# Performance work log

Hardware: AMD Instinct MI355X
Metric: run time of the kernel (lower is better)

## Reference

```python
import jax, jax.numpy as jnp
import numpy as np

B, T = 512, 512
NQ, K, M, DK, DV, DF = 1000, 5, 50, 64, 256, 50
ABILITY_SCALE = 3.0


def setup_inputs() -> dict:
    key = jax.random.key(0)
    ks = jax.random.split(key, 16)
    s = 0.05
    p = {}
    p["q_data"] = jax.random.randint(ks[0], (B, T), 0, NQ + 1)
    p["r_data"] = jax.random.randint(ks[1], (B, T), 0, K)
    p["q_embed_W"] = jax.random.normal(ks[2], (NQ + 1, DK)) * s
    p["Mk"] = jax.random.normal(ks[3], (M, DK)) * s
    p["Mv0"] = jax.random.normal(ks[4], (M, DV)) * s
    p["value_W"] = jax.random.normal(ks[5], (2 * NQ, DV)) * s
    p["value_b"] = jnp.zeros((DV,))
    p["erase_W"] = jax.random.normal(ks[6], (DV, DV)) * s
    p["erase_b"] = jnp.zeros((DV,))
    p["add_W"] = jax.random.normal(ks[7], (DV, DV)) * s
    p["add_b"] = jnp.zeros((DV,))
    p["summary_W"] = jax.random.normal(ks[8], (DV + DK, DF)) * s
    p["summary_b"] = jnp.zeros((DF,))
    p["ability_W"] = jax.random.normal(ks[9], (DF, 1)) * s
    p["ability_b"] = jnp.zeros((1,))
    p["thresh_W"] = jax.random.normal(ks[10], (DK, K - 1)) * s
    p["thresh_b"] = jnp.zeros((K - 1,))
    p["disc_W"] = jax.random.normal(ks[11], (DF + DK, 1)) * s
    p["disc_b"] = jnp.zeros((1,))
    p["corn_W"] = jax.random.normal(ks[12], (DF + DK, K - 1)) * s
    p["corn_b"] = jnp.zeros((K - 1,))
    return p


def reference(q_data, r_data, q_embed_W, Mk, Mv0, value_W, value_b, erase_W, erase_b,
              add_W, add_b, summary_W, summary_b, ability_W, ability_b,
              thresh_W, thresh_b, disc_W, disc_b, corn_W, corn_b):
    nq = value_W.shape[0] // 2
    k_cats = corn_W.shape[1] + 1
    b = q_data.shape[0]
    qe = q_embed_W[q_data]                                # [B,T,DK] question key embedding
    valid = (q_data > 0)[..., None]                       # q==0 is padding (one-hot col dropped)
    idx = jnp.maximum(q_data - 1, 0)
    # ordered embedding [one_hot(q), (r/(K-1))*one_hot(q)] @ value_W == exact row gather
    rs = r_data.astype(qe.dtype) / (k_cats - 1)
    ve = value_W[idx] + rs[..., None] * value_W[nq + idx]
    ve = jnp.where(valid, ve, 0.0) + value_b              # [B,T,DV]
    # attention over key memory (time-independent, hoisted out of the recurrence)
    w = jax.nn.softmax(jnp.einsum('btk,mk->btm', qe, Mk), axis=-1)  # [B,T,M]
    erase = jax.nn.sigmoid(ve @ erase_W + erase_b)        # [B,T,DV]
    add = jnp.tanh(ve @ add_W + add_b)                    # [B,T,DV]
    Mv_init = jnp.broadcast_to(Mv0, (b,) + Mv0.shape)     # [B,M,DV]

    def step(Mv, inp):
        w_t, e_t, a_t = inp                               # [B,M], [B,DV], [B,DV]
        read = jnp.einsum('bm,bmv->bv', w_t, Mv)          # read BEFORE write (t reads state < t)
        Mv = Mv * (1.0 - w_t[:, :, None] * e_t[:, None, :]) + w_t[:, :, None] * a_t[:, None, :]
        return Mv, read

    _, reads = jax.lax.scan(step, Mv_init,
                            (jnp.swapaxes(w, 0, 1), jnp.swapaxes(erase, 0, 1), jnp.swapaxes(add, 0, 1)))
    reads = jnp.swapaxes(reads, 0, 1)                     # [B,T,DV]

    summary = jnp.tanh(jnp.concatenate([reads, qe], -1) @ summary_W + summary_b)  # [B,T,DF]
    theta = (summary @ ability_W + ability_b)[..., 0] * ABILITY_SCALE             # [B,T]
    betas = qe @ thresh_W + thresh_b                                              # [B,T,K-1]
    di = jnp.concatenate([summary, qe], -1)                                       # [B,T,DF+DK]
    alpha = jax.nn.softplus(di @ disc_W + disc_b)[..., 0]                         # [B,T]
    logits = di @ corn_W + corn_b                                                 # [B,T,K-1]
    # CORN: cumulative conditional probs -> class probabilities
    cp = jnp.cumprod(jax.nn.sigmoid(logits), axis=-1)     # P(y > k)
    upper = jnp.concatenate([jnp.ones_like(cp[..., :1]), cp], -1)
    lower = jnp.concatenate([cp, jnp.zeros_like(cp[..., :1])], -1)
    probs = upper - lower                                 # [B,T,K]
    return theta, betas, alpha, probs, logits
```

## Files before the change

### kernel.cpp

```cpp
#include <hip/hip_runtime.h>

typedef unsigned short u16;
typedef unsigned int u32;
typedef __bf16 bf16x8 __attribute__((ext_vector_type(8)));
typedef float fx4 __attribute__((ext_vector_type(4)));
typedef float fx2 __attribute__((ext_vector_type(2)));

#define NT 262144
#define B_SZ 512
#define T_LEN 512
#define NQv 1000
#define VE_ROWS 5120
#define TLP 264
#define SSP 53

__device__ __forceinline__ float bf2f(u16 u) { return __uint_as_float(((u32)u) << 16); }
__device__ __forceinline__ u16 f2bf(float f) {
    u32 x = __float_as_uint(f);
    x += 0x7fffu + ((x >> 16) & 1u);
    return (u16)(x >> 16);
}
__device__ __forceinline__ u32 pack2(float a, float b) {
    return (u32)f2bf(a) | ((u32)f2bf(b) << 16);
}
__device__ __forceinline__ float sigm(float x) { return 1.0f / (1.0f + __expf(-x)); }
__device__ __forceinline__ float tanh_fast(float x) {
    float e2 = __expf(2.0f * x);
    return 1.0f - 2.0f / (e2 + 1.0f);
}
__device__ __forceinline__ void load_lds16(const void* g, void* l) {
    __builtin_amdgcn_global_load_lds(
        (const __attribute__((address_space(1))) u32*)g,
        (__attribute__((address_space(3))) u32*)l, 16, 0, 0);
}

__global__ __launch_bounds__(256) void k_prep_w(const float* __restrict__ eW,
                                                const float* __restrict__ aW,
                                                const float* __restrict__ sW,
                                                u16* __restrict__ Wt,
                                                u16* __restrict__ SWt) {
    int id = blockIdx.x * 256 + threadIdx.x;
    if (id < 131072) {
        int n = id >> 8, k = id & 255;
        Wt[n * 256 + k] = f2bf((n < 256) ? eW[k * 256 + n] : aW[k * 256 + (n - 256)]);
    } else {
        int id2 = id - 131072;
        if (id2 < 16384) {
            int n = id2 >> 8, k = id2 & 255;
            SWt[n * 256 + k] = (n < 50) ? f2bf(sW[k * 50 + n]) : (u16)0;
        }
    }
}

__global__ __launch_bounds__(256) void k_w_tab(const float* __restrict__ qeW,
                                               const float* __restrict__ Mk,
                                               float* __restrict__ w_tab) {
    __shared__ __align__(16) float mk[3200];
    int tid = threadIdx.x;
    for (int i = tid; i < 3200; i += 256) mk[i] = Mk[i];
    int q = blockIdx.x * 256 + tid;
    __syncthreads();
    if (q > NQv) return;

    float qe[64];
    {
        const float4* qr = (const float4*)(qeW + (size_t)q * 64);
#pragma unroll
        for (int i = 0; i < 16; i++) {
            float4 u = qr[i];
            qe[4 * i + 0] = u.x; qe[4 * i + 1] = u.y;
            qe[4 * i + 2] = u.z; qe[4 * i + 3] = u.w;
        }
    }
    float lg[50];
#pragma unroll
    for (int m = 0; m < 50; m++) {
        const float* mr = &mk[m * 64];
        float acc = 0.f;
#pragma unroll
        for (int k = 0; k < 64; k++) acc = fmaf(qe[k], mr[k], acc);
        lg[m] = acc;
    }
    float mx = -1e30f;
#pragma unroll
    for (int m = 0; m < 50; m++) mx = fmaxf(mx, lg[m]);
    float sum = 0.f;
#pragma unroll
    for (int m = 0; m < 50; m++) { lg[m] = __expf(lg[m] - mx); sum += lg[m]; }
    float inv = 1.0f / sum;
#pragma unroll
    for (int m = 0; m < 50; m++) w_tab[(size_t)q * 50 + m] = lg[m] * inv;
}

__global__ __launch_bounds__(256) void k_ve_tab(const float* __restrict__ vW,
                                                const float* __restrict__ vb,
                                                u16* __restrict__ ve_tab) {
    int id = blockIdx.x * 256 + threadIdx.x;
    int row = id >> 5, seg = id & 31;
    if (row >= VE_ROWS) return;
    int q = row / 5;
    int r = row - q * 5;
    if (q > NQv) q = NQv;
    int idx = (q > 0) ? (q - 1) : 0;
    float rs = (float)r * 0.25f;
    float vf = (q > 0) ? 1.0f : 0.0f;

    const float* pa = vW + (size_t)idx * 256 + seg * 8;
    const float* pb = pa + NQv * 256;
    float4 a0 = ((const float4*)pa)[0];
    float4 a1 = ((const float4*)pa)[1];
    float4 b0 = ((const float4*)pb)[0];
    float4 b1 = ((const float4*)pb)[1];
    const float* vbp = vb + seg * 8;
    float o0 = vf * fmaf(rs, b0.x, a0.x) + vbp[0];
    float o1 = vf * fmaf(rs, b0.y, a0.y) + vbp[1];
    float o2 = vf * fmaf(rs, b0.z, a0.z) + vbp[2];
    float o3 = vf * fmaf(rs, b0.w, a0.w) + vbp[3];
    float o4 = vf * fmaf(rs, b1.x, a1.x) + vbp[4];
    float o5 = vf * fmaf(rs, b1.y, a1.y) + vbp[5];
    float o6 = vf * fmaf(rs, b1.z, a1.z) + vbp[6];
    float o7 = vf * fmaf(rs, b1.w, a1.w) + vbp[7];
    uint4 o;
    o.x = pack2(o0, o1); o.y = pack2(o2, o3);
    o.z = pack2(o4, o5); o.w = pack2(o6, o7);
    *(uint4*)(ve_tab + (size_t)row * 256 + seg * 8) = o;
}

__global__ __launch_bounds__(256) void k_q_tabs(const float* __restrict__ qeW,
                                                const float* __restrict__ sW,
                                                const float* __restrict__ tW,
                                                const float* __restrict__ tb,
                                                const float* __restrict__ dW,
                                                const float* __restrict__ cW,
                                                float* __restrict__ sq_tab,
                                                float* __restrict__ beta_tab,
                                                float* __restrict__ dq_tab,
                                                float* __restrict__ cq_tab) {
    int id = blockIdx.x * 256 + threadIdx.x;
    int q = id >> 6, n = id & 63;
    if (q > NQv) return;
    float qe[64];
    const float4* qr = (const float4*)(qeW + (size_t)q * 64);
#pragma unroll
    for (int i = 0; i < 16; i++) {
        float4 u = qr[i];
        qe[4 * i + 0] = u.x; qe[4 * i + 1] = u.y;
        qe[4 * i + 2] = u.z; qe[4 * i + 3] = u.w;
    }
    if (n < 50) {
        float acc = 0.f;
#pragma unroll
        for (int k = 0; k < 64; k++) acc = fmaf(qe[k], sW[(256 + k) * 50 + n], acc);
        sq_tab[(size_t)q * 50 + n] = acc;
    } else if (n < 54) {
        int j = n - 50;
        float acc = tb[j];
#pragma unroll
        for (int k = 0; k < 64; k++) acc = fmaf(qe[k], tW[k * 4 + j], acc);
        beta_tab[(size_t)q * 4 + j] = acc;
    } else if (n == 54) {
        float acc = 0.f;
#pragma unroll
        for (int k = 0; k < 64; k++) acc = fmaf(qe[k], dW[50 + k], acc);
        dq_tab[q] = acc;
    } else if (n >= 56 && n < 60) {
        int j = n - 56;
        float acc = 0.f;
#pragma unroll
        for (int k = 0; k < 64; k++) acc = fmaf(qe[k], cW[(50 + k) * 4 + j], acc);
        cq_tab[(size_t)q * 4 + j] = acc;
    }
}

__global__ __launch_bounds__(256) void k_gemm_ea(const u16* __restrict__ ve,
                                                 const u16* __restrict__ Wt,
                                                 const float* __restrict__ eb,
                                                 const float* __restrict__ ab,
                                                 u16* __restrict__ e_out,
                                                 u16* __restrict__ a_out) {
    __shared__ __align__(16) u16 smem[8192];
    u16* lA = smem;
    u16* lB = smem + 4096;

    int tid = threadIdx.x;
    int row0 = blockIdx.x * 128;
    int col0 = blockIdx.y * 128;

    int wave = tid >> 6, lane = tid & 63;
    int wm = wave >> 1, wn = wave & 1;
    int rl = lane & 15, quad = lane >> 4;
    fx4 acc[4][4] = {};

    int c0 = tid, c1 = tid + 256;
    int r0_ = c0 >> 2, j0 = c0 & 3;
    int r1_ = c1 >> 2, j1 = c1 & 3;

    for (int k0 = 0; k0 < 256; k0 += 32) {
        load_lds16(ve + (size_t)(row0 + r0_) * 256 + k0 + j0 * 8, lA + c0 * 8);
        load_lds16(ve + (size_t)(row0 + r1_) * 256 + k0 + j1 * 8, lA + c1 * 8);
        load_lds16(Wt + (size_t)(col0 + r0_) * 256 + k0 + j0 * 8, lB + c0 * 8);
        load_lds16(Wt + (size_t)(col0 + r1_) * 256 + k0 + j1 * 8, lB + c1 * 8);
        __syncthreads();
        bf16x8 af[4], bfr[4];
#pragma unroll
        for (int i = 0; i < 4; i++) af[i] = *(const bf16x8*)(lA + (wm * 64 + i * 16 + rl) * 32 + quad * 8);
#pragma unroll
        for (int j = 0; j < 4; j++) bfr[j] = *(const bf16x8*)(lB + (wn * 64 + j * 16 + rl) * 32 + quad * 8);
#pragma unroll
        for (int i = 0; i < 4; i++)
#pragma unroll
            for (int j = 0; j < 4; j++)
                acc[i][j] = __builtin_amdgcn_mfma_f32_16x16x32_bf16(af[i], bfr[j], acc[i][j], 0, 0, 0);
        __syncthreads();
    }

    bool is_er = (col0 < 256);
    const float* bias = is_er ? eb : ab;
    u16* outp = is_er ? e_out : a_out;
    int cb0 = col0 & 255;
    u16* cst = smem;
#pragma unroll
    for (int h = 0; h < 2; h++) {
        if (wm == h) {
#pragma unroll
            for (int j = 0; j < 4; j++) {
                int nl = wn * 64 + j * 16 + rl;
                float bv = bias[cb0 + nl];
#pragma unroll
                for (int i = 0; i < 4; i++) {
                    int rowl = i * 16 + quad * 4;
#pragma unroll
                    for (int r = 0; r < 4; r++) {
                        float x = acc[i][j][r] + bv;
                        cst[(rowl + r) * 128 + nl] = f2bf(is_er ? sigm(x) : tanh_fast(x));
                    }
                }
            }
        }
        __syncthreads();
#pragma unroll
        for (int c = 0; c < 4; c++) {
            int idx = c * 256 + tid;
            int row = idx >> 4, seg = idx & 15;
            *(uint4*)(outp + (size_t)(row0 + h * 64 + row) * 256 + cb0 + seg * 8) =
                *(const uint4*)(cst + row * 128 + seg * 8);
        }
        __syncthreads();
    }
}

__global__ __launch_bounds__(256) void k_fused(const int* __restrict__ q_data,
                                               const int* __restrict__ r_data,
                                               const float* __restrict__ w_tab,
                                               const u16* __restrict__ e_tab,
                                               const u16* __restrict__ a_tab,
                                               const float* __restrict__ Mv0,
                                               const u16* __restrict__ SWt,
                                               const float* __restrict__ sq_tab,
                                               const float* __restrict__ sb,
                                               const float* __restrict__ abilW,
                                               const float* __restrict__ abilb,
                                               const float* __restrict__ beta_tab,
                                               const float* __restrict__ dW,
                                               const float* __restrict__ db,
                                               const float* __restrict__ dq_tab,
                                               const float* __restrict__ cW,
                                               const float* __restrict__ cb,
                                               const float* __restrict__ cq_tab,
                                               float* __restrict__ out) {
    int b = blockIdx.x;
    int tid = threadIdx.x;
    __shared__ __align__(16) u16 tileA[128 * TLP];
    __shared__ float wls[2][8][52];
    __shared__ int sq_idx[128];

    const int* qp = q_data + (size_t)b * T_LEN;
    const int* rp = r_data + (size_t)b * T_LEN;

    int wave = tid >> 6, lane = tid & 63;
    int wm = wave >> 1, wn = wave & 1;
    int rl = lane & 15, quad = lane >> 4;

    fx2 Mv[25];
#pragma unroll
    for (int i = 0; i < 25; i++) {
        Mv[i].x = Mv0[(2 * i) * 256 + tid];
        Mv[i].y = Mv0[(2 * i + 1) * 256 + tid];
    }

    u16 eu[8], au[8];
#pragma unroll
    for (int s = 0; s < 8; s++) {
        int qr = qp[s] * 5 + rp[s];
        eu[s] = e_tab[(size_t)qr * 256 + tid];
        au[s] = a_tab[(size_t)qr * 256 + tid];
    }
    if (tid < 200) {
        int s = tid / 25, m2 = tid % 25;
        float2 w0 = ((const float2*)(w_tab + (size_t)qp[s] * 50))[m2];
        wls[0][s][2 * m2] = w0.x;
        wls[0][s][2 * m2 + 1] = w0.y;
    }
    __syncthreads();

    const int ngrp = T_LEN / 8;
    for (int g = 0; g < ngrp; g++) {
        int cur = g & 1, nxt = cur ^ 1;
        bool has_next = (g + 1 < ngrp);
        int tn0 = (g + 1) * 8;

        u16 eun[8], aun[8];
        float2 wn_ = make_float2(0.f, 0.f);
        if (has_next) {
#pragma unroll
            for (int s = 0; s < 8; s++) {
                int qr = qp[tn0 + s] * 5 + rp[tn0 + s];
                eun[s] = e_tab[(size_t)qr * 256 + tid];
                aun[s] = a_tab[(size_t)qr * 256 + tid];
            }
            if (tid < 200) {
                int s = tid / 25, m2 = tid % 25;
                wn_ = ((const float2*)(w_tab + (size_t)qp[tn0 + s] * 50))[m2];
            }
        }

#pragma unroll
        for (int s = 0; s < 8; s++) {
            float e = bf2f(eu[s]), a = bf2f(au[s]);
            fx2 e2; e2.x = e; e2.y = e;
            fx2 a2; a2.x = a; a2.y = a;
            const fx2* wv = (const fx2*)&wls[cur][s][0];
            fx2 rd2; rd2.x = 0.f; rd2.y = 0.f;
#pragma unroll
            for (int i = 0; i < 25; i++) {
                fx2 w2 = wv[i];
                rd2 = rd2 + w2 * Mv[i];
                fx2 t2 = a2 - e2 * Mv[i];
                Mv[i] = Mv[i] + w2 * t2;
            }
            int tokrow = (g * 8 + s) & 127;
            tileA[tokrow * TLP + tid] = f2bf(rd2.x + rd2.y);
        }

        if (has_next) {
            if (tid < 200) {
                int s = tid / 25, m2 = tid % 25;
                wls[nxt][s][2 * m2] = wn_.x;
                wls[nxt][s][2 * m2 + 1] = wn_.y;
            }
#pragma unroll
            for (int s = 0; s < 8; s++) { eu[s] = eun[s]; au[s] = aun[s]; }
        }
        __syncthreads();

        if ((g & 15) == 15) {
            int tile0 = (g >> 4) * 128;
            if (tid < 128) sq_idx[tid] = qp[tile0 + tid];

            fx4 acc[4][2] = {};
#pragma unroll
            for (int ks = 0; ks < 8; ks++) {
                int k0 = ks * 32;
                bf16x8 af[4], bfr[2];
#pragma unroll
                for (int i = 0; i < 4; i++)
                    af[i] = *(const bf16x8*)(tileA + (wm * 64 + i * 16 + rl) * TLP + k0 + quad * 8);
#pragma unroll
                for (int j = 0; j < 2; j++)
                    bfr[j] = *(const bf16x8*)(SWt + (size_t)(wn * 32 + j * 16 + rl) * 256 + k0 + quad * 8);
#pragma unroll
                for (int i = 0; i < 4; i++)
#pragma unroll
                    for (int j = 0; j < 2; j++)
                        acc[i][j] = __builtin_amdgcn_mfma_f32_16x16x32_bf16(af[i], bfr[j], acc[i][j], 0, 0, 0);
            }
            __syncthreads();

            float* sS = (float*)tileA;
#pragma unroll
            for (int j = 0; j < 2; j++) {
                int n = wn * 32 + j * 16 + rl;
                if (n < 50) {
#pragma unroll
                    for (int i = 0; i < 4; i++) {
                        int rowl = wm * 64 + i * 16 + quad * 4;
#pragma unroll
                        for (int r = 0; r < 4; r++)
                            sS[(rowl + r) * SSP + n] = acc[i][j][r];
                    }
                }
            }
            __syncthreads();

            if (tid < 128) {
                int q = sq_idx[tid];
                size_t gtok = (size_t)b * T_LEN + tile0 + tid;
                const float* sq = sq_tab + (size_t)q * 50;
                const float* sp = sS + tid * SSP;

                float th = abilb[0];
                float da = db[0];
                float l0 = cb[0], l1 = cb[1], l2 = cb[2], l3 = cb[3];
#pragma unroll
                for (int i = 0; i < 50; i++) {
                    float sv = tanh_fast(sp[i] + sq[i] + sb[i]);
                    th = fmaf(sv, abilW[i], th);
                    da = fmaf(sv, dW[i], da);
                    l0 = fmaf(sv, cW[i * 4 + 0], l0);
                    l1 = fmaf(sv, cW[i * 4 + 1], l1);
                    l2 = fmaf(sv, cW[i * 4 + 2], l2);
                    l3 = fmaf(sv, cW[i * 4 + 3], l3);
                }
                da += dq_tab[q];
                l0 += cq_tab[q * 4 + 0];
                l1 += cq_tab[q * 4 + 1];
                l2 += cq_tab[q * 4 + 2];
                l3 += cq_tab[q * 4 + 3];

                out[gtok] = th * 3.0f;

                out[NT + gtok * 4 + 0] = beta_tab[q * 4 + 0];
                out[NT + gtok * 4 + 1] = beta_tab[q * 4 + 1];
                out[NT + gtok * 4 + 2] = beta_tab[q * 4 + 2];
                out[NT + gtok * 4 + 3] = beta_tab[q * 4 + 3];

                out[5 * (size_t)NT + gtok] = logf(1.0f + __expf(da));

                out[11 * (size_t)NT + gtok * 4 + 0] = l0;
                out[11 * (size_t)NT + gtok * 4 + 1] = l1;
                out[11 * (size_t)NT + gtok * 4 + 2] = l2;
                out[11 * (size_t)NT + gtok * 4 + 3] = l3;

                float c0 = sigm(l0);
                float c1 = c0 * sigm(l1);
                float c2 = c1 * sigm(l2);
                float c3 = c2 * sigm(l3);
                size_t pb = 6 * (size_t)NT + gtok * 5;
                out[pb + 0] = 1.0f - c0;
                out[pb + 1] = c0 - c1;
                out[pb + 2] = c1 - c2;
                out[pb + 3] = c2 - c3;
                out[pb + 4] = c3;
            }
            __syncthreads();
        }
    }
}

extern "C" void kernel_launch(void* const* d_in, const int* in_sizes, int n_in,
                              void* d_out, int out_size, void* d_ws, size_t ws_size,
                              hipStream_t stream) {
    (void)in_sizes; (void)n_in; (void)out_size; (void)ws_size;
    const int* q_data = (const int*)d_in[0];
    const int* r_data = (const int*)d_in[1];
    const float* qeW = (const float*)d_in[2];
    const float* Mk  = (const float*)d_in[3];
    const float* Mv0 = (const float*)d_in[4];
    const float* vW  = (const float*)d_in[5];
    const float* vb  = (const float*)d_in[6];
    const float* eW  = (const float*)d_in[7];
    const float* eb  = (const float*)d_in[8];
    const float* aW  = (const float*)d_in[9];
    const float* ab  = (const float*)d_in[10];
    const float* sW  = (const float*)d_in[11];
    const float* sb  = (const float*)d_in[12];
    const float* abilW = (const float*)d_in[13];
    const float* abilb = (const float*)d_in[14];
    const float* tW  = (const float*)d_in[15];
    const float* tb  = (const float*)d_in[16];
    const float* dW  = (const float*)d_in[17];
    const float* db  = (const float*)d_in[18];
    const float* cW  = (const float*)d_in[19];
    const float* cb  = (const float*)d_in[20];

    char* ws = (char*)d_ws;
    u16* Wt        = (u16*)(ws + 0);
    u16* SWt       = (u16*)(ws + 262144);
    float* w_tab   = (float*)(ws + 327680);
    float* sq_tab  = (float*)(ws + 532480);
    float* beta_tab= (float*)(ws + 737280);
    float* dq_tab  = (float*)(ws + 753664);
    float* cq_tab  = (float*)(ws + 757760);
    u16* ve_tab    = (u16*)(ws + 774144);
    u16* e_tab     = (u16*)(ws + 3395584);
    u16* a_tab     = (u16*)(ws + 6017024);
    float* out = (float*)d_out;

    k_prep_w<<<576, 256, 0, stream>>>(eW, aW, sW, Wt, SWt);
    k_w_tab<<<4, 256, 0, stream>>>(qeW, Mk, w_tab);
    k_ve_tab<<<VE_ROWS / 8, 256, 0, stream>>>(vW, vb, ve_tab);
    k_q_tabs<<<256, 256, 0, stream>>>(qeW, sW, tW, tb, dW, cW,
                                      sq_tab, beta_tab, dq_tab, cq_tab);
    dim3 g2(VE_ROWS / 128, 4);
    k_gemm_ea<<<g2, 256, 0, stream>>>(ve_tab, Wt, eb, ab, e_tab, a_tab);
    k_fused<<<B_SZ, 256, 0, stream>>>(q_data, r_data, w_tab, e_tab, a_tab, Mv0,
                                      SWt, sq_tab, sb, abilW, abilb, beta_tab,
                                      dW, db, dq_tab, cW, cb, cq_tab, out);
}
```

Before: 464.7 us.

## Merge prep kernels into one launch, keep summary weights in registers, widen LDS reads

The four small table-building kernels become one kernel that branches on block index, removing three launches and the gaps between them. In the fused recurrent kernel, the summary-weight fragments for the MFMA are loaded once into registers instead of being re-read from global memory for every 128-token tile. The memory-update loop reads attention weights as 16-byte vectors instead of 8-byte ones. Keeping the weight fragments resident adds 16 vector registers per thread, which may reduce occupancy or cause spills.

Result: slower. 654.3 us (+40.8%).

```diff
diff --git a/kernel.cpp b/kernel.cpp
--- a/kernel.cpp
+++ b/kernel.cpp
@@ -34,36 +34,47 @@
         (__attribute__((address_space(3))) u32*)l, 16, 0, 0);
 }
 
-__global__ __launch_bounds__(256) void k_prep_w(const float* __restrict__ eW,
-                                                const float* __restrict__ aW,
-                                                const float* __restrict__ sW,
-                                                u16* __restrict__ Wt,
-                                                u16* __restrict__ SWt) {
-    int id = blockIdx.x * 256 + threadIdx.x;
-    if (id < 131072) {
-        int n = id >> 8, k = id & 255;
-        Wt[n * 256 + k] = f2bf((n < 256) ? eW[k * 256 + n] : aW[k * 256 + (n - 256)]);
-    } else {
-        int id2 = id - 131072;
-        if (id2 < 16384) {
-            int n = id2 >> 8, k = id2 & 255;
-            SWt[n * 256 + k] = (n < 50) ? f2bf(sW[k * 50 + n]) : (u16)0;
-        }
-    }
-}
-
-__global__ __launch_bounds__(256) void k_w_tab(const float* __restrict__ qeW,
-                                               const float* __restrict__ Mk,
-                                               float* __restrict__ w_tab) {
-    __shared__ __align__(16) float mk[3200];
+__global__ __launch_bounds__(256) void k_prep(const float* __restrict__ eW,
+                                              const float* __restrict__ aW,
+                                              const float* __restrict__ sW,
+                                              const float* __restrict__ qeW,
+                                              const float* __restrict__ Mk,
+                                              const float* __restrict__ vW,
+                                              const float* __restrict__ vb,
+                                              const float* __restrict__ tW,
+                                              const float* __restrict__ tb,
+                                              const float* __restrict__ dW,
+                                              const float* __restrict__ cW,
+                                              u16* __restrict__ Wt,
+                                              u16* __restrict__ SWt,
+                                              float* __restrict__ w_tab,
+                                              u16* __restrict__ ve_tab,
+                                              float* __restrict__ sq_tab,
+                                              float* __restrict__ beta_tab,
+                                              float* __restrict__ dq_tab,
+                                              float* __restrict__ cq_tab) {
+    int bid = blockIdx.x;
     int tid = threadIdx.x;
-    for (int i = tid; i < 3200; i += 256) mk[i] = Mk[i];
-    int q = blockIdx.x * 256 + tid;
-    __syncthreads();
-    if (q > NQv) return;
-
-    float qe[64];
-    {
+
+    if (bid < 576) {
+        int id = bid * 256 + tid;
+        if (id < 131072) {
+            int n = id >> 8, k = id & 255;
+            Wt[n * 256 + k] = f2bf((n < 256) ? eW[k * 256 + n] : aW[k * 256 + (n - 256)]);
+        } else {
+            int id2 = id - 131072;
+            if (id2 < 16384) {
+                int n = id2 >> 8, k = id2 & 255;
+                SWt[n * 256 + k] = (n < 50) ? f2bf(sW[k * 50 + n]) : (u16)0;
+            }
+        }
+    } else if (bid < 580) {
+        __shared__ __align__(16) float mk[3200];
+        for (int i = tid; i < 3200; i += 256) mk[i] = Mk[i];
+        int q = (bid - 576) * 256 + tid;
+        __syncthreads();
+        if (q > NQv) return;
+        float qe[64];
         const float4* qr = (const float4*)(qeW + (size_t)q * 64);
 #pragma unroll
         for (int i = 0; i < 16; i++) {
@@ -71,104 +82,88 @@
             qe[4 * i + 0] = u.x; qe[4 * i + 1] = u.y;
             qe[4 * i + 2] = u.z; qe[4 * i + 3] = u.w;
         }
-    }
-    float lg[50];
-#pragma unroll
-    for (int m = 0; m < 50; m++) {
-        const float* mr = &mk[m * 64];
-        float acc = 0.f;
-#pragma unroll
-        for (int k = 0; k < 64; k++) acc = fmaf(qe[k], mr[k], acc);
-        lg[m] = acc;
-    }
-    float mx = -1e30f;
-#pragma unroll
-    for (int m = 0; m < 50; m++) mx = fmaxf(mx, lg[m]);
-    float sum = 0.f;
-#pragma unroll
-    for (int m = 0; m < 50; m++) { lg[m] = __expf(lg[m] - mx); sum += lg[m]; }
-    float inv = 1.0f / sum;
-#pragma unroll
-    for (int m = 0; m < 50; m++) w_tab[(size_t)q * 50 + m] = lg[m] * inv;
-}
-
-__global__ __launch_bounds__(256) void k_ve_tab(const float* __restrict__ vW,
-                                                const float* __restrict__ vb,
-                                                u16* __restrict__ ve_tab) {
-    int id = blockIdx.x * 256 + threadIdx.x;
-    int row = id >> 5, seg = id & 31;
-    if (row >= VE_ROWS) return;
-    int q = row / 5;
-    int r = row - q * 5;
-    if (q > NQv) q = NQv;
-    int idx = (q > 0) ? (q - 1) : 0;
-    float rs = (float)r * 0.25f;
-    float vf = (q > 0) ? 1.0f : 0.0f;
-
-    const float* pa = vW + (size_t)idx * 256 + seg * 8;
-    const float* pb = pa + NQv * 256;
-    float4 a0 = ((const float4*)pa)[0];
-    float4 a1 = ((const float4*)pa)[1];
-    float4 b0 = ((const float4*)pb)[0];
-    float4 b1 = ((const float4*)pb)[1];
-    const float* vbp = vb + seg * 8;
-    float o0 = vf * fmaf(rs, b0.x, a0.x) + vbp[0];
-    float o1 = vf * fmaf(rs, b0.y, a0.y) + vbp[1];
-    float o2 = vf * fmaf(rs, b0.z, a0.z) + vbp[2];
-    float o3 = vf * fmaf(rs, b0.w, a0.w) + vbp[3];
-    float o4 = vf * fmaf(rs, b1.x, a1.x) + vbp[4];
-    float o5 = vf * fmaf(rs, b1.y, a1.y) + vbp[5];
-    float o6 = vf * fmaf(rs, b1.z, a1.z) + vbp[6];
-    float o7 = vf * fmaf(rs, b1.w, a1.w) + vbp[7];
-    uint4 o;
-    o.x = pack2(o0, o1); o.y = pack2(o2, o3);
-    o.z = pack2(o4, o5); o.w = pack2(o6, o7);
-    *(uint4*)(ve_tab + (size_t)row * 256 + seg * 8) = o;
-}
-
-__global__ __launch_bounds__(256) void k_q_tabs(const float* __restrict__ qeW,
-                                                const float* __restrict__ sW,
-                                                const float* __restrict__ tW,
-                                                const float* __restrict__ tb,
-                                                const float* __restrict__ dW,
-                                                const float* __restrict__ cW,
-                                                float* __restrict__ sq_tab,
-                                                float* __restrict__ beta_tab,
-                                                float* __restrict__ dq_tab,
-                                                float* __restrict__ cq_tab) {
-    int id = blockIdx.x * 256 + threadIdx.x;
-    int q = id >> 6, n = id & 63;
-    if (q > NQv) return;
-    float qe[64];
-    const float4* qr = (const float4*)(qeW + (size_t)q * 64);
-#pragma unroll
-    for (int i = 0; i < 16; i++) {
-        float4 u = qr[i];
-        qe[4 * i + 0] = u.x; qe[4 * i + 1] = u.y;
-        qe[4 * i + 2] = u.z; qe[4 * i + 3] = u.w;
-    }
-    if (n < 50) {
-        float acc = 0.f;
-#pragma unroll
-        for (int k = 0; k < 64; k++) acc = fmaf(qe[k], sW[(256 + k) * 50 + n], acc);
-        sq_tab[(size_t)q * 50 + n] = acc;
-    } else if (n < 54) {
-        int j = n - 50;
-        float acc = tb[j];
-#pragma unroll
-        for (int k = 0; k < 64; k++) acc = fmaf(qe[k], tW[k * 4 + j], acc);
-        beta_tab[(size_t)q * 4 + j] = acc;
-    } else if (n == 54) {
-        float acc = 0.f;
-#pragma unroll
-        for (int k = 0; k < 64; k++) acc = fmaf(qe[k], dW[50 + k], acc);
-        dq_tab[q] = acc;
-    } else if (n >= 56 && n < 60) {
-        int j = n - 56;
-        float acc = 0.f;
-#pragma unroll
-        for (int k = 0; k < 64; k++) acc = fmaf(qe[k], cW[(50 + k) * 4 + j], acc);
-        cq_tab[(size_t)q * 4 + j] = acc;
+        float lg[50];
+#pragma unroll
+        for (int m = 0; m < 50; m++) {
+            const float* mr = &mk[m * 64];
+            float acc = 0.f;
+#pragma unroll
+            for (int k = 0; k < 64; k++) acc = fmaf(qe[k], mr[k], acc);
+            lg[m] = acc;
+        }
+        float mx = -1e30f;
+#pragma unroll
+        for (int m = 0; m < 50; m++) mx = fmaxf(mx, lg[m]);
+        float sum = 0.f;
+#pragma unroll
+        for (int m = 0; m < 50; m++) { lg[m] = __expf(lg[m] - mx); sum += lg[m]; }
+        float inv = 1.0f / sum;
+#pragma unroll
+        for (int m = 0; m < 50; m++) w_tab[(size_t)q * 50 + m] = lg[m] * inv;
+    } else if (bid < 1220) {
+        int id = (bid - 580) * 256 + tid;
+        int row = id >> 5, seg = id & 31;
+        if (row >= VE_ROWS) return;
+        int q = row / 5;
+        int r = row - q * 5;
+        if (q > NQv) q = NQv;
+        int idx = (q > 0) ? (q - 1) : 0;
+        float rs = (float)r * 0.25f;
+        float vf = (q > 0) ? 1.0f : 0.0f;
+        const float* pa = vW + (size_t)idx * 256 + seg * 8;
+        const float* pb = pa + NQv * 256;
+        float4 a0 = ((const float4*)pa)[0];
+        float4 a1 = ((const float4*)pa)[1];
+        float4 b0 = ((const float4*)pb)[0];
+        float4 b1 = ((const float4*)pb)[1];
+        const float* vbp = vb + seg * 8;
+        float o0 = vf * fmaf(rs, b0.x, a0.x) + vbp[0];
+        float o1 = vf * fmaf(rs, b0.y, a0.y) + vbp[1];
+        float o2 = vf * fmaf(rs, b0.z, a0.z) + vbp[2];
+        float o3 = vf * fmaf(rs, b0.w, a0.w) + vbp[3];
+        float o4 = vf * fmaf(rs, b1.x, a1.x) + vbp[4];
+        float o5 = vf * fmaf(rs, b1.y, a1.y) + vbp[5];
+        float o6 = vf * fmaf(rs, b1.z, a1.z) + vbp[6];
+        float o7 = vf * fmaf(rs, b1.w, a1.w) + vbp[7];
+        uint4 o;
+        o.x = pack2(o0, o1); o.y = pack2(o2, o3);
+        o.z = pack2(o4, o5); o.w = pack2(o6, o7);
+        *(uint4*)(ve_tab + (size_t)row * 256 + seg * 8) = o;
+    } else {
+        int id = (bid - 1220) * 256 + tid;
+        int q = id >> 6, n = id & 63;
+        if (q > NQv) return;
+        float qe[64];
+        const float4* qr = (const float4*)(qeW + (size_t)q * 64);
+#pragma unroll
+        for (int i = 0; i < 16; i++) {
+            float4 u = qr[i];
+            qe[4 * i + 0] = u.x; qe[4 * i + 1] = u.y;
+            qe[4 * i + 2] = u.z; qe[4 * i + 3] = u.w;
+        }
+        if (n < 50) {
+            float acc = 0.f;
+#pragma unroll
+            for (int k = 0; k < 64; k++) acc = fmaf(qe[k], sW[(256 + k) * 50 + n], acc);
+            sq_tab[(size_t)q * 50 + n] = acc;
+        } else if (n < 54) {
+            int j = n - 50;
+            float acc = tb[j];
+#pragma unroll
+            for (int k = 0; k < 64; k++) acc = fmaf(qe[k], tW[k * 4 + j], acc);
+            beta_tab[(size_t)q * 4 + j] = acc;
+        } else if (n == 54) {
+            float acc = 0.f;
+#pragma unroll
+            for (int k = 0; k < 64; k++) acc = fmaf(qe[k], dW[50 + k], acc);
+            dq_tab[q] = acc;
+        } else if (n >= 56 && n < 60) {
+            int j = n - 56;
+            float acc = 0.f;
+#pragma unroll
+            for (int k = 0; k < 64; k++) acc = fmaf(qe[k], cW[(50 + k) * 4 + j], acc);
+            cq_tab[(size_t)q * 4 + j] = acc;
+        }
     }
 }
 
@@ -271,7 +266,7 @@
     int b = blockIdx.x;
     int tid = threadIdx.x;
     __shared__ __align__(16) u16 tileA[128 * TLP];
-    __shared__ float wls[2][8][52];
+    __shared__ __align__(16) float wls[2][8][52];
     __shared__ int sq_idx[128];
 
     const int* qp = q_data + (size_t)b * T_LEN;
@@ -280,6 +275,13 @@
     int wave = tid >> 6, lane = tid & 63;
     int wm = wave >> 1, wn = wave & 1;
     int rl = lane & 15, quad = lane >> 4;
+
+    bf16x8 swr[2][8];
+#pragma unroll
+    for (int j = 0; j < 2; j++)
+#pragma unroll
+        for (int ks = 0; ks < 8; ks++)
+            swr[j][ks] = *(const bf16x8*)(SWt + (size_t)(wn * 32 + j * 16 + rl) * 256 + ks * 32 + quad * 8);
 
     fx2 Mv[25];
 #pragma unroll
@@ -329,14 +331,25 @@
             float e = bf2f(eu[s]), a = bf2f(au[s]);
             fx2 e2; e2.x = e; e2.y = e;
             fx2 a2; a2.x = a; a2.y = a;
-            const fx2* wv = (const fx2*)&wls[cur][s][0];
+            const fx4* wv4 = (const fx4*)&wls[cur][s][0];
             fx2 rd2; rd2.x = 0.f; rd2.y = 0.f;
 #pragma unroll
-            for (int i = 0; i < 25; i++) {
-                fx2 w2 = wv[i];
-                rd2 = rd2 + w2 * Mv[i];
-                fx2 t2 = a2 - e2 * Mv[i];
-                Mv[i] = Mv[i] + w2 * t2;
+            for (int i = 0; i < 12; i++) {
+                fx4 w4 = wv4[i];
+                fx2 wa; wa.x = w4.x; wa.y = w4.y;
+                fx2 wb; wb.x = w4.z; wb.y = w4.w;
+                rd2 = rd2 + wa * Mv[2 * i];
+                fx2 ta = a2 - e2 * Mv[2 * i];
+                Mv[2 * i] = Mv[2 * i] + wa * ta;
+                rd2 = rd2 + wb * Mv[2 * i + 1];
+                fx2 tbp = a2 - e2 * Mv[2 * i + 1];
+                Mv[2 * i + 1] = Mv[2 * i + 1] + wb * tbp;
+            }
+            {
+                fx2 w2 = *(const fx2*)&wls[cur][s][48];
+                rd2 = rd2 + w2 * Mv[24];
+                fx2 t2 = a2 - e2 * Mv[24];
+                Mv[24] = Mv[24] + w2 * t2;
             }
             int tokrow = (g * 8 + s) & 127;
             tileA[tokrow * TLP + tid] = f2bf(rd2.x + rd2.y);
@@ -361,18 +374,15 @@
 #pragma unroll
             for (int ks = 0; ks < 8; ks++) {
                 int k0 = ks * 32;
-                bf16x8 af[4], bfr[2];
+                bf16x8 af[4];
 #pragma unroll
                 for (int i = 0; i < 4; i++)
                     af[i] = *(const bf16x8*)(tileA + (wm * 64 + i * 16 + rl) * TLP + k0 + quad * 8);
 #pragma unroll
-                for (int j = 0; j < 2; j++)
-                    bfr[j] = *(const bf16x8*)(SWt + (size_t)(wn * 32 + j * 16 + rl) * 256 + k0 + quad * 8);
-#pragma unroll
                 for (int i = 0; i < 4; i++)
 #pragma unroll
                     for (int j = 0; j < 2; j++)
-                        acc[i][j] = __builtin_amdgcn_mfma_f32_16x16x32_bf16(af[i], bfr[j], acc[i][j], 0, 0, 0);
+                        acc[i][j] = __builtin_amdgcn_mfma_f32_16x16x32_bf16(af[i], swr[j][ks], acc[i][j], 0, 0, 0);
             }
             __syncthreads();
 
@@ -486,11 +496,9 @@
     u16* a_tab     = (u16*)(ws + 6017024);
     float* out = (float*)d_out;
 
-    k_prep_w<<<576, 256, 0, stream>>>(eW, aW, sW, Wt, SWt);
-    k_w_tab<<<4, 256, 0, stream>>>(qeW, Mk, w_tab);
-    k_ve_tab<<<VE_ROWS / 8, 256, 0, stream>>>(vW, vb, ve_tab);
-    k_q_tabs<<<256, 256, 0, stream>>>(qeW, sW, tW, tb, dW, cW,
-                                      sq_tab, beta_tab, dq_tab, cq_tab);
+    k_prep<<<1476, 256, 0, stream>>>(eW, aW, sW, qeW, Mk, vW, vb, tW, tb, dW, cW,
+                                     Wt, SWt, w_tab, ve_tab,
+                                     sq_tab, beta_tab, dq_tab, cq_tab);
     dim3 g2(VE_ROWS / 128, 4);
     k_gemm_ea<<<g2, 256, 0, stream>>>(ve_tab, Wt, eb, ab, e_tab, a_tab);
     k_fused<<<B_SZ, 256, 0, stream>>>(q_data, r_data, w_tab, e_tab, a_tab, Mv0,
```
